# Kernel optimization log

Measured on AMD Instinct MI355X. Metric: run time of the kernel, lower is better.

The kernel has to match this reference:

```python
import jax, jax.numpy as jnp
import numpy as np

B, N, C = 8, 1568, 768
H = 12
D = C // H  # 64
EPS = 1e-12  # torch F.normalize default eps


def setup_inputs() -> dict:
    key = jax.random.key(0)
    k1, k2, k3 = jax.random.split(key, 3)
    x = jax.random.normal(k1, (B, N, C), dtype=jnp.float32)
    W_qkv = jax.random.normal(k2, (3 * C, C), dtype=jnp.float32) * 0.02
    b_qkv = jax.random.normal(k3, (3 * C,), dtype=jnp.float32) * 0.02
    return {"x": x, "W_qkv": W_qkv, "b_qkv": b_qkv}


def _l2norm(t):
    # matches torch.nn.functional.normalize(t, dim=-1): x / max(||x||, eps)
    n = jnp.sqrt(jnp.sum(t * t, axis=-1, keepdims=True))
    return t / jnp.maximum(n, EPS)


def reference(x, W_qkv, b_qkv):
    b, n, c = x.shape
    qkv = x @ W_qkv.T + b_qkv                      # [B, N, 3C]
    qkv = qkv.reshape(b, n, 3, H, D)
    qkv = jnp.transpose(qkv, (2, 0, 3, 1, 4))      # [3, B, H, N, D]
    q, k, v = qkv[0], qkv[1], qkv[2]
    attn = jnp.einsum('bhnd,bhmd->bhnm', _l2norm(q), _l2norm(k))  # cosine sims
    attn = jax.nn.softmax(attn, axis=-1)
    out = jnp.einsum('bhnm,bhmd->bhnd', attn, v)   # [B, H, N, D]
    out = jnp.transpose(out, (0, 2, 1, 3)).reshape(b, n, c)
    return out
```

## Files before the change

### kernel.cpp

```cpp
#include <hip/hip_runtime.h>

typedef __attribute__((ext_vector_type(8))) short bf16x8;
typedef __attribute__((ext_vector_type(4))) float f32x4;
typedef __attribute__((ext_vector_type(16))) float f32x16;
typedef __attribute__((ext_vector_type(4))) short short4v;

namespace {
constexpr int B = 8;
constexpr int N = 1568;
constexpr int NP = 1664;
constexpr int C = 768;
constexpr int H = 12;
constexpr int D = 64;
constexpr int M = B * N;
constexpr int NT = 25;
constexpr int QT = 13;
constexpr size_t QKP = (size_t)B * H * NP * D;
constexpr size_t OFF_XB = 0;
constexpr size_t OFF_WB = OFF_XB + (size_t)M * C;
constexpr size_t OFF_Q  = OFF_WB + (size_t)3 * C * C;
constexpr size_t OFF_K  = OFF_Q + QKP;
constexpr size_t OFF_VT = OFF_K + QKP;
constexpr float LOG2E = 1.44269504088896f;
}

__device__ __forceinline__ ushort f2bf(float f) {
    union { float f; unsigned u; } a; a.f = f;
    unsigned u = a.u;
    u += 0x7FFF + ((u >> 16) & 1);
    return (ushort)(u >> 16);
}
__device__ __forceinline__ void gload16(const ushort* g, ushort* l) {
    __builtin_amdgcn_global_load_lds(
        (const __attribute__((address_space(1))) ushort*)g,
        (__attribute__((address_space(3))) ushort*)l, 16, 0, 0);
}
__device__ __forceinline__ unsigned cvtpk(float lo, float hi) {
    unsigned r;
    asm("v_cvt_pk_bf16_f32 %0, %1, %2" : "=v"(r) : "v"(lo), "v"(hi));
    return r;
}
__device__ __forceinline__ void plswap(unsigned &a, unsigned &b) {
    asm("v_permlane32_swap_b32 %0, %1" : "+v"(a), "+v"(b));
}

__global__ __launch_bounds__(256) void cvt_bf16_kernel(
    const float* __restrict__ x, const float* __restrict__ W,
    ushort* __restrict__ xb, ushort* __restrict__ wb)
{
    constexpr int NX = M * C / 4;
    constexpr int NW = 3 * C * C / 4;
    for (int i = blockIdx.x * blockDim.x + threadIdx.x; i < NX + NW;
         i += gridDim.x * blockDim.x) {
        float4 v; ushort* dst; int o;
        if (i < NX) { v = ((const float4*)x)[i]; dst = xb; o = i; }
        else        { v = ((const float4*)W)[i - NX]; dst = wb; o = i - NX; }
        short4v s;
        s.x = (short)f2bf(v.x); s.y = (short)f2bf(v.y);
        s.z = (short)f2bf(v.z); s.w = (short)f2bf(v.w);
        *(short4v*)(dst + (size_t)o * 4) = s;
    }
}

__global__ __launch_bounds__(256) void qkv_mfma_kernel(
    const ushort* __restrict__ xb, const ushort* __restrict__ Wb,
    const float* __restrict__ bias, ushort* __restrict__ qg,
    ushort* __restrict__ kg, ushort* __restrict__ vtg)
{
    __shared__ __align__(16) ushort Ab[128][64];
    __shared__ __align__(16) ushort Bb[128][64];

    const int tid = threadIdx.x;
    const int l = tid & 63;
    const int w = tid >> 6;
    const int l15 = l & 15, lg = l >> 4;

    const int orig = blockIdx.x;
    const int xcd = orig & 7;
    const int base = (xcd < 4) ? xcd * 221 : 4 * 221 + (xcd - 4) * 220;
    const int wgid = base + (orig >> 3);
    const int mt = wgid / 18;
    const int jt = wgid - mt * 18;
    const int m0 = mt * 128;
    const int j0 = jt * 128;

    const int wr = w >> 1, wc = w & 1;
    const int Rr = l >> 3;
    const int cch = l & 7;

    f32x4 acc[4][4] = {};

    for (int kb = 0; kb < C; kb += 64) {
        __syncthreads();
        #pragma unroll
        for (int i = 0; i < 4; ++i) {
            const int R = (w * 4 + i) * 8 + Rr;
            const int cg = (cch ^ (R & 7)) * 8;
            gload16(xb + (size_t)(m0 + R) * C + kb + cg, &Ab[0][0] + (w * 4 + i) * 512);
            gload16(Wb + (size_t)(j0 + R) * C + kb + cg, &Bb[0][0] + (w * 4 + i) * 512);
        }
        __syncthreads();

        #pragma unroll
        for (int kk = 0; kk < 2; ++kk) {
            bf16x8 af[4], bfr[4];
            #pragma unroll
            for (int t = 0; t < 4; ++t) {
                const int ra = wr * 64 + t * 16 + l15;
                af[t]  = *(const bf16x8*)&Ab[ra][((kk * 4 + lg) ^ (ra & 7)) * 8];
                const int rb = wc * 64 + t * 16 + l15;
                bfr[t] = *(const bf16x8*)&Bb[rb][((kk * 4 + lg) ^ (rb & 7)) * 8];
            }
            #pragma unroll
            for (int mi = 0; mi < 4; ++mi)
                #pragma unroll
                for (int nj = 0; nj < 4; ++nj)
                    acc[mi][nj] = __builtin_amdgcn_mfma_f32_16x16x32_bf16(
                        af[mi], bfr[nj], acc[mi][nj], 0, 0, 0);
        }
    }

    const int sel = jt / 6;
    if (sel < 2) {
        ushort* dst = (sel == 0) ? qg : kg;
        const float scl = (sel == 0) ? LOG2E : 1.f;
        const int jbase = j0 + wc * 64;
        const int h = (jbase - sel * C) >> 6;
        float bbv[4];
        #pragma unroll
        for (int nj = 0; nj < 4; ++nj) bbv[nj] = bias[jbase + nj * 16 + l15];
        #pragma unroll
        for (int mi = 0; mi < 4; ++mi) {
            #pragma unroll
            for (int r = 0; r < 4; ++r) {
                const float v0 = acc[mi][0][r] + bbv[0];
                const float v1 = acc[mi][1][r] + bbv[1];
                const float v2 = acc[mi][2][r] + bbv[2];
                const float v3 = acc[mi][3][r] + bbv[3];
                float ssq = v0*v0 + v1*v1 + v2*v2 + v3*v3;
                ssq += __shfl_xor(ssq, 1); ssq += __shfl_xor(ssq, 2);
                ssq += __shfl_xor(ssq, 4); ssq += __shfl_xor(ssq, 8);
                const float inv = scl / fmaxf(sqrtf(ssq), 1e-12f);
                const int m = m0 + wr * 64 + mi * 16 + lg * 4 + r;
                const int b_ = m / N, n_ = m - b_ * N;
                ushort* o = dst + (((size_t)b_ * H + h) * NP + n_) * D + l15;
                o[0]  = f2bf(v0 * inv);
                o[16] = f2bf(v1 * inv);
                o[32] = f2bf(v2 * inv);
                o[48] = f2bf(v3 * inv);
            }
        }
    } else {
        #pragma unroll
        for (int nj = 0; nj < 4; ++nj) {
            const int jcol = j0 + wc * 64 + nj * 16 + l15;
            const int rem = jcol - 2 * C;
            const int h = rem >> 6, d = rem & 63;
            const float bb = bias[jcol];
            #pragma unroll
            for (int mi = 0; mi < 4; ++mi) {
                const int mb = m0 + wr * 64 + mi * 16 + lg * 4;
                const int b_ = mb / N, n_ = mb - b_ * N;
                short4v o;
                o.x = (short)f2bf(acc[mi][nj][0] + bb);
                o.y = (short)f2bf(acc[mi][nj][1] + bb);
                o.z = (short)f2bf(acc[mi][nj][2] + bb);
                o.w = (short)f2bf(acc[mi][nj][3] + bb);
                *(short4v*)&vtg[(((size_t)b_ * H + h) * D + d) * NP + n_] = o;
            }
        }
    }
}

__global__ __launch_bounds__(256) void attn_kernel(
    const ushort* __restrict__ qg, const ushort* __restrict__ kg,
    const ushort* __restrict__ vtg, float* __restrict__ out)
{
    __shared__ __align__(16) ushort KsB[2][64 * 64];
    __shared__ __align__(16) ushort VtB[2][64 * 64];

    const int tid = threadIdx.x;
    const int l   = tid & 63;
    const int w   = tid >> 6;
    const int l31 = l & 31;
    const int hi  = l >> 5;

    const int bid = blockIdx.x;
    const int grp = bid >> 3;
    const int qt  = grp % QT;
    const int bh  = (bid & 7) + 8 * (grp / QT);

    const ushort* qp  = qg  + (size_t)bh * NP * D;
    const ushort* kp  = kg  + (size_t)bh * NP * D;
    const ushort* vtp = vtg + (size_t)bh * D * NP;

    const int rsub = l >> 3;
    const int cg   = ((l & 7) ^ rsub) << 3;

    bf16x8 qf[4];
    {
        const ushort* qr = qp + (size_t)(qt * 128 + w * 32 + l31) * D + hi * 8;
        #pragma unroll
        for (int ds = 0; ds < 4; ++ds)
            qf[ds] = *(const bf16x8*)(qr + ds * 16);
    }

    #pragma unroll
    for (int p = 0; p < 2; ++p) {
        const int rb = p * 32 + w * 8;
        gload16(kp + (size_t)(rb + rsub) * D + cg, KsB[0] + rb * 64);
        gload16(vtp + (size_t)(rb + rsub) * NP + cg, VtB[0] + rb * 64);
    }
    __syncthreads();

    f32x16 o_acc[2] = {};
    float denom = 0.f;
    int cur = 0;

    for (int kt = 0; kt < NT; ++kt) {
        if (kt + 1 < NT) {
            ushort* Kn = KsB[cur ^ 1];
            ushort* Vn = VtB[cur ^ 1];
            #pragma unroll
            for (int p = 0; p < 2; ++p) {
                const int rb = p * 32 + w * 8;
                gload16(kp + (size_t)((kt + 1) * 64 + rb + rsub) * D + cg, Kn + rb * 64);
                gload16(vtp + (size_t)(rb + rsub) * NP + (kt + 1) * 64 + cg, Vn + rb * 64);
            }
        }
        const ushort* Kc = KsB[cur];
        const ushort* Vc = VtB[cur];

        unsigned pw[16];
        #pragma unroll
        for (int f = 0; f < 2; ++f) {
            if (f == 1 && kt == NT - 1) {
                #pragma unroll
                for (int i = 0; i < 8; ++i) pw[8 + i] = 0;
            } else {
                f32x16 st = {};
                __builtin_amdgcn_s_setprio(1);
                #pragma unroll
                for (int ds = 0; ds < 4; ++ds) {
                    const int krow = f * 32 + l31;
                    const int ch = (2 * ds + hi) ^ (krow & 7);
                    const bf16x8 kf = *(const bf16x8*)(Kc + krow * 64 + ch * 8);
                    st = __builtin_amdgcn_mfma_f32_32x32x16_bf16(kf, qf[ds], st, 0, 0, 0);
                }
                __builtin_amdgcn_s_setprio(0);
                float p[16];
                #pragma unroll
                for (int r = 0; r < 16; ++r) p[r] = __builtin_amdgcn_exp2f(st[r]);
                const float t =
                    (((p[0]+p[1])+(p[2]+p[3])) + ((p[4]+p[5])+(p[6]+p[7]))) +
                    (((p[8]+p[9])+(p[10]+p[11])) + ((p[12]+p[13])+(p[14]+p[15])));
                denom += t;
                #pragma unroll
                for (int i = 0; i < 8; ++i)
                    pw[f * 8 + i] = cvtpk(p[2 * i], p[2 * i + 1]);
            }
        }

        #pragma unroll
        for (int q4 = 0; q4 < 4; ++q4) {
            plswap(pw[q4 * 4 + 0], pw[q4 * 4 + 2]);
            plswap(pw[q4 * 4 + 1], pw[q4 * 4 + 3]);
        }

        __builtin_amdgcn_s_setprio(1);
        #pragma unroll
        for (int dt = 0; dt < 2; ++dt) {
            #pragma unroll
            for (int ks = 0; ks < 4; ++ks) {
                const int vrow = dt * 32 + l31;
                const int ch = (2 * ks + hi) ^ (vrow & 7);
                const bf16x8 vf = *(const bf16x8*)(Vc + vrow * 64 + ch * 8);
                union { unsigned u[4]; bf16x8 v; } A;
                A.u[0] = pw[ks * 4 + 0]; A.u[1] = pw[ks * 4 + 1];
                A.u[2] = pw[ks * 4 + 2]; A.u[3] = pw[ks * 4 + 3];
                o_acc[dt] = __builtin_amdgcn_mfma_f32_32x32x16_bf16(
                    A.v, vf, o_acc[dt], 0, 0, 0);
            }
        }
        __builtin_amdgcn_s_setprio(0);

        __syncthreads();
        cur ^= 1;
    }

    denom += __shfl_xor(denom, 32);
    float* dn = (float*)&KsB[0][0];
    if (hi == 0) dn[w * 32 + l31] = 1.f / denom;
    __syncthreads();

    const int b_ = bh / H;
    const int h_ = bh % H;
    #pragma unroll
    for (int g = 0; g < 4; ++g) {
        const f32x4 inv4 = *(const f32x4*)&dn[w * 32 + g * 8 + hi * 4];
        #pragma unroll
        for (int r3 = 0; r3 < 4; ++r3) {
            const int n = qt * 128 + w * 32 + g * 8 + hi * 4 + r3;
            if (n < N) {
                const float iv = inv4[r3];
                #pragma unroll
                for (int dt = 0; dt < 2; ++dt)
                    out[((size_t)b_ * N + n) * C + (h_ << 6) + dt * 32 + l31] =
                        o_acc[dt][g * 4 + r3] * iv;
            }
        }
    }
}

extern "C" void kernel_launch(void* const* d_in, const int* in_sizes, int n_in,
                              void* d_out, int out_size, void* d_ws, size_t ws_size,
                              hipStream_t stream) {
    const float* x  = (const float*)d_in[0];
    const float* Wq = (const float*)d_in[1];
    const float* bq = (const float*)d_in[2];
    float* out = (float*)d_out;
    ushort* ws = (ushort*)d_ws;

    ushort* xb  = ws + OFF_XB;
    ushort* wb  = ws + OFF_WB;
    ushort* qg  = ws + OFF_Q;
    ushort* kg  = ws + OFF_K;
    ushort* vtg = ws + OFF_VT;

    cvt_bf16_kernel<<<2048, 256, 0, stream>>>(x, Wq, xb, wb);
    qkv_mfma_kernel<<<(M / 128) * (3 * C / 128), 256, 0, stream>>>(xb, wb, bq, qg, kg, vtg);
    attn_kernel<<<QT * B * H, 256, 0, stream>>>(qg, kg, vtg, out);
}
```

Measured before the change: 171.8 us.

## Double KV tile size to 128 rows per pipeline stage

```diff
diff --git a/kernel.cpp b/kernel.cpp
--- a/kernel.cpp
+++ b/kernel.cpp
@@ -13,8 +13,8 @@
 constexpr int H = 12;
 constexpr int D = 64;
 constexpr int M = B * N;
-constexpr int NT = 25;
 constexpr int QT = 13;
+constexpr int KT2 = 13;
 constexpr size_t QKP = (size_t)B * H * NP * D;
 constexpr size_t OFF_XB = 0;
 constexpr size_t OFF_WB = OFF_XB + (size_t)M * C;
@@ -176,8 +176,8 @@
     const ushort* __restrict__ qg, const ushort* __restrict__ kg,
     const ushort* __restrict__ vtg, float* __restrict__ out)
 {
-    __shared__ __align__(16) ushort KsB[2][64 * 64];
-    __shared__ __align__(16) ushort VtB[2][64 * 64];
+    __shared__ __align__(16) ushort KsB[2][128 * 64];
+    __shared__ __align__(16) ushort VtB[2][2][64 * 64];
 
     const int tid = threadIdx.x;
     const int l   = tid & 63;
@@ -206,43 +206,54 @@
     }
 
     #pragma unroll
-    for (int p = 0; p < 2; ++p) {
+    for (int p = 0; p < 4; ++p) {
         const int rb = p * 32 + w * 8;
         gload16(kp + (size_t)(rb + rsub) * D + cg, KsB[0] + rb * 64);
-        gload16(vtp + (size_t)(rb + rsub) * NP + cg, VtB[0] + rb * 64);
-    }
+    }
+    #pragma unroll
+    for (int h2 = 0; h2 < 2; ++h2)
+        #pragma unroll
+        for (int p = 0; p < 2; ++p) {
+            const int rb = p * 32 + w * 8;
+            gload16(vtp + (size_t)(rb + rsub) * NP + h2 * 64 + cg,
+                    VtB[0][h2] + rb * 64);
+        }
     __syncthreads();
 
     f32x16 o_acc[2] = {};
     float denom = 0.f;
     int cur = 0;
 
-    for (int kt = 0; kt < NT; ++kt) {
-        if (kt + 1 < NT) {
+    for (int kt = 0; kt < KT2 - 1; ++kt) {
+        {
             ushort* Kn = KsB[cur ^ 1];
-            ushort* Vn = VtB[cur ^ 1];
-            #pragma unroll
-            for (int p = 0; p < 2; ++p) {
+            #pragma unroll
+            for (int p = 0; p < 4; ++p) {
                 const int rb = p * 32 + w * 8;
-                gload16(kp + (size_t)((kt + 1) * 64 + rb + rsub) * D + cg, Kn + rb * 64);
-                gload16(vtp + (size_t)(rb + rsub) * NP + (kt + 1) * 64 + cg, Vn + rb * 64);
-            }
+                gload16(kp + (size_t)((kt + 1) * 128 + rb + rsub) * D + cg, Kn + rb * 64);
+            }
+            #pragma unroll
+            for (int h2 = 0; h2 < 2; ++h2)
+                #pragma unroll
+                for (int p = 0; p < 2; ++p) {
+                    const int rb = p * 32 + w * 8;
+                    gload16(vtp + (size_t)(rb + rsub) * NP + (kt + 1) * 128 + h2 * 64 + cg,
+                            VtB[cur ^ 1][h2] + rb * 64);
+                }
         }
         const ushort* Kc = KsB[cur];
-        const ushort* Vc = VtB[cur];
-
-        unsigned pw[16];
-        #pragma unroll
-        for (int f = 0; f < 2; ++f) {
-            if (f == 1 && kt == NT - 1) {
-                #pragma unroll
-                for (int i = 0; i < 8; ++i) pw[8 + i] = 0;
-            } else {
+
+        #pragma unroll
+        for (int h2 = 0; h2 < 2; ++h2) {
+            unsigned pw[16];
+            #pragma unroll
+            for (int f01 = 0; f01 < 2; ++f01) {
+                const int fr = h2 * 2 + f01;
                 f32x16 st = {};
                 __builtin_amdgcn_s_setprio(1);
                 #pragma unroll
                 for (int ds = 0; ds < 4; ++ds) {
-                    const int krow = f * 32 + l31;
+                    const int krow = fr * 32 + l31;
                     const int ch = (2 * ds + hi) ^ (krow & 7);
                     const bf16x8 kf = *(const bf16x8*)(Kc + krow * 64 + ch * 8);
                     st = __builtin_amdgcn_mfma_f32_32x32x16_bf16(kf, qf[ds], st, 0, 0, 0);
@@ -257,16 +268,71 @@
                 denom += t;
                 #pragma unroll
                 for (int i = 0; i < 8; ++i)
-                    pw[f * 8 + i] = cvtpk(p[2 * i], p[2 * i + 1]);
-            }
-        }
-
+                    pw[f01 * 8 + i] = cvtpk(p[2 * i], p[2 * i + 1]);
+            }
+
+            #pragma unroll
+            for (int q4 = 0; q4 < 4; ++q4) {
+                plswap(pw[q4 * 4 + 0], pw[q4 * 4 + 2]);
+                plswap(pw[q4 * 4 + 1], pw[q4 * 4 + 3]);
+            }
+
+            const ushort* Vc = VtB[cur][h2];
+            __builtin_amdgcn_s_setprio(1);
+            #pragma unroll
+            for (int dt = 0; dt < 2; ++dt) {
+                #pragma unroll
+                for (int ks = 0; ks < 4; ++ks) {
+                    const int vrow = dt * 32 + l31;
+                    const int ch = (2 * ks + hi) ^ (vrow & 7);
+                    const bf16x8 vf = *(const bf16x8*)(Vc + vrow * 64 + ch * 8);
+                    union { unsigned u[4]; bf16x8 v; } A;
+                    A.u[0] = pw[ks * 4 + 0]; A.u[1] = pw[ks * 4 + 1];
+                    A.u[2] = pw[ks * 4 + 2]; A.u[3] = pw[ks * 4 + 3];
+                    o_acc[dt] = __builtin_amdgcn_mfma_f32_32x32x16_bf16(
+                        A.v, vf, o_acc[dt], 0, 0, 0);
+                }
+            }
+            __builtin_amdgcn_s_setprio(0);
+        }
+
+        __syncthreads();
+        cur ^= 1;
+    }
+
+    {
+        const ushort* Kc = KsB[cur];
+        unsigned pw[16];
+        {
+            f32x16 st = {};
+            __builtin_amdgcn_s_setprio(1);
+            #pragma unroll
+            for (int ds = 0; ds < 4; ++ds) {
+                const int krow = l31;
+                const int ch = (2 * ds + hi) ^ (krow & 7);
+                const bf16x8 kf = *(const bf16x8*)(Kc + krow * 64 + ch * 8);
+                st = __builtin_amdgcn_mfma_f32_32x32x16_bf16(kf, qf[ds], st, 0, 0, 0);
+            }
+            __builtin_amdgcn_s_setprio(0);
+            float p[16];
+            #pragma unroll
+            for (int r = 0; r < 16; ++r) p[r] = __builtin_amdgcn_exp2f(st[r]);
+            const float t =
+                (((p[0]+p[1])+(p[2]+p[3])) + ((p[4]+p[5])+(p[6]+p[7]))) +
+                (((p[8]+p[9])+(p[10]+p[11])) + ((p[12]+p[13])+(p[14]+p[15])));
+            denom += t;
+            #pragma unroll
+            for (int i = 0; i < 8; ++i)
+                pw[i] = cvtpk(p[2 * i], p[2 * i + 1]);
+        }
+        #pragma unroll
+        for (int i = 0; i < 8; ++i) pw[8 + i] = 0;
         #pragma unroll
         for (int q4 = 0; q4 < 4; ++q4) {
             plswap(pw[q4 * 4 + 0], pw[q4 * 4 + 2]);
             plswap(pw[q4 * 4 + 1], pw[q4 * 4 + 3]);
         }
-
+        const ushort* Vc = VtB[cur][0];
         __builtin_amdgcn_s_setprio(1);
         #pragma unroll
         for (int dt = 0; dt < 2; ++dt) {
@@ -283,12 +349,10 @@
             }
         }
         __builtin_amdgcn_s_setprio(0);
-
-        __syncthreads();
-        cur ^= 1;
     }
 
     denom += __shfl_xor(denom, 32);
+    __syncthreads();
     float* dn = (float*)&KsB[0][0];
     if (hi == 0) dn[w * 32 + l31] = 1.f / denom;
     __syncthreads();
```

Result: slower. 175.3 us (+2.0%).
